# Kernel optimization log

Hardware: AMD Instinct MI355X
Metric: run time of the kernel (lower is better)

## Reference

```python
import jax, jax.numpy as jnp
import numpy as np

B, H = 16384, 1024
EPS = 1e-5


def setup_inputs() -> dict:
    key = jax.random.key(0)
    ks = jax.random.split(key, 12)
    inp = {
        "t": 0,
        "h": jax.random.normal(ks[0], (B, H), jnp.float32),
        "e": jax.random.normal(ks[1], (B, H), jnp.float32),
        # LiquidNeuron params
        "W_rec": jax.random.normal(ks[2], (H, H), jnp.float32) * 0.1,
        "bias": jnp.zeros((H,), jnp.float32),
        "tau": jnp.ones((H,), jnp.float32),
        "decay": jnp.ones((H,), jnp.float32),
        "ln_w": jnp.ones((H,), jnp.float32),
        "ln_b": jnp.zeros((H,), jnp.float32),
        # context_encoder: Linear -> ReLU -> Linear (dropout = identity in eval)
        "ce_w1": jax.random.normal(ks[3], (H, H), jnp.float32) * (1.0 / np.sqrt(H)),
        "ce_b1": jnp.zeros((H,), jnp.float32),
        "ce_w2": jax.random.normal(ks[4], (H, H), jnp.float32) * (1.0 / np.sqrt(H)),
        "ce_b2": jnp.zeros((H,), jnp.float32),
        # param_modulator
        "pm_w": jax.random.normal(ks[5], (H, H), jnp.float32) * (1.0 / np.sqrt(H)),
        "pm_b": jnp.zeros((H,), jnp.float32),
    }
    return inp


def reference(t, h, e, W_rec, bias, tau, decay, ln_w, ln_b,
              ce_w1, ce_b1, ce_w2, ce_b2, pm_w, pm_b):
    # context encoder (eval mode: dropout is identity)
    context = jnp.maximum(h @ ce_w1.T + ce_b1, 0.0) @ ce_w2.T + ce_b2  # [B,H]
    pa = context @ pm_w.T + pm_b  # param_adjustment [B,H]
    # bmm(e[:,None,:], (W_rec*(1+pa)[:,:,None]).T) == (1+pa) * (e @ W_rec.T)
    matmul_result = (1.0 + pa) * (e @ W_rec.T)  # [B,H]
    tau_adjusted = tau * jax.nn.sigmoid(pa)  # [B,H]
    dh_dt = (-decay * h + matmul_result + bias) / tau_adjusted
    # LayerNorm over last dim
    mu = jnp.mean(dh_dt, axis=-1, keepdims=True)
    var = jnp.var(dh_dt, axis=-1, keepdims=True)
    dh_dt = (dh_dt - mu) * jax.lax.rsqrt(var + EPS) * ln_w + ln_b
    return dh_dt
```

## Files before the change

kernel.cpp:

```cpp
#include <hip/hip_runtime.h>
#include <stdint.h>

#define H_DIM 1024
#define B_DIM 16384

typedef unsigned short u16;
typedef short bf16x8 __attribute__((ext_vector_type(8)));
typedef float f32x4 __attribute__((ext_vector_type(4)));

__device__ __forceinline__ u16 f2bf(float f) {
  union { float f; uint32_t u; } v; v.f = f;
  uint32_t r = v.u + 0x7fffu + ((v.u >> 16) & 1u);
  return (u16)(r >> 16);
}

#define GLDS16(gsrc, ldst)                                                                 \
  __builtin_amdgcn_global_load_lds((const __attribute__((address_space(1))) void*)(gsrc),  \
                                   (__attribute__((address_space(3))) void*)(ldst), 16, 0, 0)

__global__ __launch_bounds__(256) void cvt_f32_bf16(const float* __restrict__ in,
                                                    u16* __restrict__ out, int n4) {
  int i = blockIdx.x * blockDim.x + threadIdx.x;
  const int stride = gridDim.x * blockDim.x;
  const float4* __restrict__ in4 = (const float4*)in;
  ushort4* __restrict__ out4 = (ushort4*)out;
  for (; i < n4; i += stride) {
    float4 v = in4[i];
    ushort4 o;
    o.x = f2bf(v.x); o.y = f2bf(v.y); o.z = f2bf(v.z); o.w = f2bf(v.w);
    out4[i] = o;
  }
}


template <int MODE>
__device__ __forceinline__ void subtile_step(u16* shp, int slot, int slot2, int aoff, int boff,
                                             int wv, const u16*& pA0, const u16*& pA1,
                                             const u16*& pB0, const u16*& pB1,
                                             f32x4 (&acc)[8][4]) {
  const u16* Ab = shp + slot * 16384 + aoff;
  const u16* Bb = shp + slot * 16384 + 8192 + boff;
  bf16x8 aF[4], bF[4];
#pragma unroll
  for (int i = 0; i < 4; ++i) aF[i] = *(const bf16x8*)(Ab + i * 512);
#pragma unroll
  for (int i = 0; i < 4; ++i) bF[i] = *(const bf16x8*)(Bb + i * 512);
  if (MODE == 2) {
    u16* d = shp + slot2 * 16384 + wv * 1024;
    GLDS16(pA0, d); GLDS16(pA1, d + 512);
    pA0 += 32; pA1 += 32;
  }
  __builtin_amdgcn_s_barrier();
  asm volatile("s_waitcnt lgkmcnt(0)" ::: "memory");
  __builtin_amdgcn_s_setprio(1);
#pragma unroll
  for (int mf = 0; mf < 4; ++mf)
#pragma unroll
    for (int nf = 0; nf < 4; ++nf)
      acc[mf][nf] = __builtin_amdgcn_mfma_f32_16x16x32_bf16(aF[mf], bF[nf], acc[mf][nf], 0, 0, 0);
  __builtin_amdgcn_s_setprio(0);
  __builtin_amdgcn_s_barrier();
#pragma unroll
  for (int i = 0; i < 4; ++i) aF[i] = *(const bf16x8*)(Ab + (4 + i) * 512);
  if (MODE == 2) {
    u16* d = shp + slot2 * 16384 + 8192 + wv * 1024;
    GLDS16(pB0, d); GLDS16(pB1, d + 512);
    pB0 += 32; pB1 += 32;
  }
  __builtin_amdgcn_s_barrier();
  asm volatile("s_waitcnt lgkmcnt(0)" ::: "memory");
  __builtin_amdgcn_s_setprio(1);
#pragma unroll
  for (int mf = 0; mf < 4; ++mf)
#pragma unroll
    for (int nf = 0; nf < 4; ++nf)
      acc[4 + mf][nf] =
          __builtin_amdgcn_mfma_f32_16x16x32_bf16(aF[mf], bF[nf], acc[4 + mf][nf], 0, 0, 0);
  __builtin_amdgcn_s_setprio(0);
  if (MODE == 2) asm volatile("s_waitcnt vmcnt(4)" ::: "memory");
  if (MODE == 1) asm volatile("s_waitcnt vmcnt(0)" ::: "memory");
  __builtin_amdgcn_s_barrier();
}

template <bool RELU, bool HASBIAS, typename OUT>
__global__ __launch_bounds__(512, 2) void gemm256(const u16* __restrict__ A,
                                                  const u16* __restrict__ W,
                                                  const float* __restrict__ bias,
                                                  OUT* __restrict__ C) {
  extern __shared__ u16 sh[];
  const int t = threadIdx.x;
  const int wv = t >> 6, l = t & 63;
  const int wm = wv >> 2, wn = wv & 3;
  const int l15 = l & 15, lg = l >> 4;

  const int bid = blockIdx.x;
  const int logical = (bid & 7) * 32 + (bid >> 3);
  const int m0 = (logical >> 2) * 256;
  const int n0 = (logical & 3) * 256;

  const int koff = (lg ^ ((l15 >> 1) & 3)) * 8;
  const int aoff = (wm * 128 + l15) * 32 + koff;
  const int boff = (wn * 64 + l15) * 32 + koff;

  const int rowst = wv * 32 + (l >> 2);
  const int ksl = ((l & 3) ^ ((l >> 3) & 3)) * 8;
  const u16* pA0 = A + (size_t)(m0 + rowst) * H_DIM + ksl;
  const u16* pA1 = pA0 + 16 * H_DIM;
  const u16* pB0 = W + (size_t)(n0 + rowst) * H_DIM + ksl;
  const u16* pB1 = pB0 + 16 * H_DIM;

  f32x4 acc[8][4] = {};

  { u16* d = sh + wv * 1024;                 GLDS16(pA0, d); GLDS16(pA1, d + 512); pA0 += 32; pA1 += 32; }
  { u16* d = sh + 8192 + wv * 1024;          GLDS16(pB0, d); GLDS16(pB1, d + 512); pB0 += 32; pB1 += 32; }
  { u16* d = sh + 16384 + wv * 1024;         GLDS16(pA0, d); GLDS16(pA1, d + 512); pA0 += 32; pA1 += 32; }
  { u16* d = sh + 16384 + 8192 + wv * 1024;  GLDS16(pB0, d); GLDS16(pB1, d + 512); pB0 += 32; pB1 += 32; }
  asm volatile("s_waitcnt vmcnt(4)" ::: "memory");
  __builtin_amdgcn_s_barrier();

  for (int s = 0; s < 30; ++s)
    subtile_step<2>(sh, s & 3, (s + 2) & 3, aoff, boff, wv, pA0, pA1, pB0, pB1, acc);
  subtile_step<1>(sh, 2, 0, aoff, boff, wv, pA0, pA1, pB0, pB1, acc);
  subtile_step<0>(sh, 3, 0, aoff, boff, wv, pA0, pA1, pB0, pB1, acc);

  float bv[4];
#pragma unroll
  for (int nf = 0; nf < 4; ++nf)
    bv[nf] = HASBIAS ? bias[n0 + wn * 64 + nf * 16 + l15] : 0.0f;
#pragma unroll
  for (int mf = 0; mf < 8; ++mf) {
#pragma unroll
    for (int nf = 0; nf < 4; ++nf) {
      const int col = n0 + wn * 64 + nf * 16 + l15;
#pragma unroll
      for (int j = 0; j < 4; ++j) {
        const int row = m0 + wm * 128 + mf * 16 + lg * 4 + j;
        float v = acc[mf][nf][j] + bv[nf];
        if (RELU) v = fmaxf(v, 0.0f);
        if constexpr (sizeof(OUT) == 2)
          C[(size_t)row * H_DIM + col] = (OUT)f2bf(v);
        else
          C[(size_t)row * H_DIM + col] = v;
      }
    }
  }
}

__global__ __launch_bounds__(256) void liquid_ln(const float* __restrict__ h,
                                                 const float* __restrict__ pa,
                                                 const float* __restrict__ ev,
                                                 const float* __restrict__ bias,
                                                 const float* __restrict__ tau,
                                                 const float* __restrict__ decay,
                                                 const float* __restrict__ lnw,
                                                 const float* __restrict__ lnb,
                                                 float* __restrict__ out) {
  const int row = blockIdx.x;
  const int t = threadIdx.x;
  const size_t base = (size_t)row * H_DIM + t * 4;
  const int pcol = t * 4;

  float hf[4], pf[4], ef[4], bf_[4], tf[4], df[4];
  *(float4*)hf = *(const float4*)(h + base);
  *(float4*)pf = *(const float4*)(pa + base);
  *(float4*)ef = *(const float4*)(ev + base);
  *(float4*)bf_ = *(const float4*)(bias + pcol);
  *(float4*)tf = *(const float4*)(tau + pcol);
  *(float4*)df = *(const float4*)(decay + pcol);

  float d[4], s = 0.f, ss = 0.f;
#pragma unroll
  for (int j = 0; j < 4; ++j) {
    const float sig = 1.0f / (1.0f + __expf(-pf[j]));
    const float num = fmaf(-df[j], hf[j], fmaf(1.0f + pf[j], ef[j], bf_[j]));
    const float val = num / (tf[j] * sig);
    d[j] = val;
    s += val;
    ss += val * val;
  }
#pragma unroll
  for (int off = 32; off > 0; off >>= 1) {
    s += __shfl_down(s, off);
    ss += __shfl_down(ss, off);
  }
  __shared__ float rs[4], rss[4];
  const int wv = t >> 6;
  if ((t & 63) == 0) { rs[wv] = s; rss[wv] = ss; }
  __syncthreads();
  const float S = rs[0] + rs[1] + rs[2] + rs[3];
  const float SS = rss[0] + rss[1] + rss[2] + rss[3];
  const float mu = S * (1.0f / H_DIM);
  const float var = SS * (1.0f / H_DIM) - mu * mu;
  const float rstd = rsqrtf(var + 1e-5f);

  float lw[4], lb[4], o[4];
  *(float4*)lw = *(const float4*)(lnw + pcol);
  *(float4*)lb = *(const float4*)(lnb + pcol);
#pragma unroll
  for (int j = 0; j < 4; ++j) o[j] = fmaf((d[j] - mu) * rstd, lw[j], lb[j]);
  *(float4*)(out + base) = *(float4*)o;
}

extern "C" void kernel_launch(void* const* d_in, const int* in_sizes, int n_in,
                              void* d_out, int out_size, void* d_ws, size_t ws_size,
                              hipStream_t stream) {
  const float* h = (const float*)d_in[1];
  const float* e = (const float*)d_in[2];
  const float* Wrec = (const float*)d_in[3];
  const float* bias = (const float*)d_in[4];
  const float* tau = (const float*)d_in[5];
  const float* decay = (const float*)d_in[6];
  const float* lnw = (const float*)d_in[7];
  const float* lnb = (const float*)d_in[8];
  const float* ce_w1 = (const float*)d_in[9];
  const float* ce_b1 = (const float*)d_in[10];
  const float* ce_w2 = (const float*)d_in[11];
  const float* ce_b2 = (const float*)d_in[12];
  const float* pm_w = (const float*)d_in[13];
  const float* pm_b = (const float*)d_in[14];
  float* out = (float*)d_out;

  char* ws = (char*)d_ws;
  const size_t MB = 1024 * 1024;
  u16* w1b = (u16*)(ws + 0 * MB);
  u16* w2b = (u16*)(ws + 2 * MB);
  u16* w3b = (u16*)(ws + 4 * MB);
  u16* w4b = (u16*)(ws + 6 * MB);
  u16* ebf = (u16*)(ws + 8 * MB);
  u16* hbf = (u16*)(ws + 40 * MB);
  u16* t1 = (u16*)(ws + 72 * MB);
  u16* ctx = (u16*)(ws + 104 * MB);
  float* paf = (float*)(ws + 40 * MB);
  float* evf = (float*)(ws + 104 * MB);

  const int nBH4 = (B_DIM * H_DIM) / 4;
  const int nHH4 = (H_DIM * H_DIM) / 4;
  cvt_f32_bf16<<<2048, 256, 0, stream>>>(h, hbf, nBH4);
  cvt_f32_bf16<<<2048, 256, 0, stream>>>(e, ebf, nBH4);
  cvt_f32_bf16<<<512, 256, 0, stream>>>(ce_w1, w1b, nHH4);
  cvt_f32_bf16<<<512, 256, 0, stream>>>(ce_w2, w2b, nHH4);
  cvt_f32_bf16<<<512, 256, 0, stream>>>(pm_w, w3b, nHH4);
  cvt_f32_bf16<<<512, 256, 0, stream>>>(Wrec, w4b, nHH4);

  const int LDS_BYTES = 131072;
  hipFuncSetAttribute((const void*)gemm256<true, true, u16>,
                      hipFuncAttributeMaxDynamicSharedMemorySize, LDS_BYTES);
  hipFuncSetAttribute((const void*)gemm256<false, true, u16>,
                      hipFuncAttributeMaxDynamicSharedMemorySize, LDS_BYTES);
  hipFuncSetAttribute((const void*)gemm256<false, true, float>,
                      hipFuncAttributeMaxDynamicSharedMemorySize, LDS_BYTES);
  hipFuncSetAttribute((const void*)gemm256<false, false, float>,
                      hipFuncAttributeMaxDynamicSharedMemorySize, LDS_BYTES);

  const int NWG = (B_DIM / 256) * (H_DIM / 256);
  gemm256<true, true, u16><<<NWG, 512, LDS_BYTES, stream>>>(hbf, w1b, ce_b1, t1);
  gemm256<false, true, u16><<<NWG, 512, LDS_BYTES, stream>>>(t1, w2b, ce_b2, ctx);
  gemm256<false, true, float><<<NWG, 512, LDS_BYTES, stream>>>(ctx, w3b, pm_b, paf);
  gemm256<false, false, float><<<NWG, 512, LDS_BYTES, stream>>>(ebf, w4b, nullptr, evf);

  liquid_ln<<<B_DIM, 256, 0, stream>>>(h, paf, evf, bias, tau, decay, lnw, lnb, out);
}
```

Measured before the change: 251.2 us.

## Deepen GEMM prefetch to three stages, fuse weight casts, one-wave-per-row LayerNorm

The GEMM main loop now prefetches three K-slices ahead instead of two. It issues A and B loads together once per step and does all 32 MFMAs between a single pair of barriers, which removes the mid-step barrier and lgkmcnt wait. The four weight conversions are merged into one launch. The LayerNorm kernel maps one wavefront to each row and reduces with xor shuffles, so no shared-memory reduction or block sync is needed. Risks: more live fragment registers with 8 A fragments, and the removed lgkmcnt wait relies on the compiler to insert LDS read waits. Each LN lane's 16 contiguous floats are read as four float4 loads at a 64-byte lane stride, which is less coalesced.

```diff
diff --git a/kernel.cpp b/kernel.cpp
--- a/kernel.cpp
+++ b/kernel.cpp
@@ -32,51 +32,63 @@
   }
 }
 
+__global__ __launch_bounds__(256) void cvt4_f32_bf16(const float* __restrict__ a0,
+                                                     const float* __restrict__ a1,
+                                                     const float* __restrict__ a2,
+                                                     const float* __restrict__ a3,
+                                                     u16* __restrict__ o0, u16* __restrict__ o1,
+                                                     u16* __restrict__ o2, u16* __restrict__ o3) {
+  const int which = blockIdx.x >> 8;
+  const float* in = which == 0 ? a0 : which == 1 ? a1 : which == 2 ? a2 : a3;
+  u16* out = which == 0 ? o0 : which == 1 ? o1 : which == 2 ? o2 : o3;
+  const int n4 = (H_DIM * H_DIM) / 4;
+  int i = (blockIdx.x & 255) * 256 + threadIdx.x;
+  const float4* in4 = (const float4*)in;
+  ushort4* out4 = (ushort4*)out;
+  for (; i < n4; i += 256 * 256) {
+    float4 v = in4[i];
+    ushort4 o;
+    o.x = f2bf(v.x); o.y = f2bf(v.y); o.z = f2bf(v.z); o.w = f2bf(v.w);
+    out4[i] = o;
+  }
+}
+
 
 template <int MODE>
-__device__ __forceinline__ void subtile_step(u16* shp, int slot, int slot2, int aoff, int boff,
+__device__ __forceinline__ void subtile_step(u16* shp, int slot, int slot3, int aoff, int boff,
                                              int wv, const u16*& pA0, const u16*& pA1,
                                              const u16*& pB0, const u16*& pB1,
                                              f32x4 (&acc)[8][4]) {
   const u16* Ab = shp + slot * 16384 + aoff;
   const u16* Bb = shp + slot * 16384 + 8192 + boff;
-  bf16x8 aF[4], bF[4];
+  bf16x8 aF[8], bF[4];
 #pragma unroll
   for (int i = 0; i < 4; ++i) aF[i] = *(const bf16x8*)(Ab + i * 512);
 #pragma unroll
   for (int i = 0; i < 4; ++i) bF[i] = *(const bf16x8*)(Bb + i * 512);
-  if (MODE == 2) {
-    u16* d = shp + slot2 * 16384 + wv * 1024;
-    GLDS16(pA0, d); GLDS16(pA1, d + 512);
-    pA0 += 32; pA1 += 32;
+#pragma unroll
+  for (int i = 4; i < 8; ++i) aF[i] = *(const bf16x8*)(Ab + i * 512);
+  if (MODE == 3) {
+    u16* da = shp + slot3 * 16384 + wv * 1024;
+    GLDS16(pA0, da); GLDS16(pA1, da + 512);
+    u16* db = shp + slot3 * 16384 + 8192 + wv * 1024;
+    GLDS16(pB0, db); GLDS16(pB1, db + 512);
+    pA0 += 32; pA1 += 32; pB0 += 32; pB1 += 32;
   }
   __builtin_amdgcn_s_barrier();
-  asm volatile("s_waitcnt lgkmcnt(0)" ::: "memory");
   __builtin_amdgcn_s_setprio(1);
 #pragma unroll
   for (int mf = 0; mf < 4; ++mf)
+#pragma unroll
+    for (int nf = 0; nf < 4; ++nf)
+      acc[mf][nf] = __builtin_amdgcn_mfma_f32_16x16x32_bf16(aF[mf], bF[nf], acc[mf][nf], 0, 0, 0);
+#pragma unroll
+  for (int mf = 4; mf < 8; ++mf)
 #pragma unroll
     for (int nf = 0; nf < 4; ++nf)
       acc[mf][nf] = __builtin_amdgcn_mfma_f32_16x16x32_bf16(aF[mf], bF[nf], acc[mf][nf], 0, 0, 0);
   __builtin_amdgcn_s_setprio(0);
-  __builtin_amdgcn_s_barrier();
-#pragma unroll
-  for (int i = 0; i < 4; ++i) aF[i] = *(const bf16x8*)(Ab + (4 + i) * 512);
-  if (MODE == 2) {
-    u16* d = shp + slot2 * 16384 + 8192 + wv * 1024;
-    GLDS16(pB0, d); GLDS16(pB1, d + 512);
-    pB0 += 32; pB1 += 32;
-  }
-  __builtin_amdgcn_s_barrier();
-  asm volatile("s_waitcnt lgkmcnt(0)" ::: "memory");
-  __builtin_amdgcn_s_setprio(1);
-#pragma unroll
-  for (int mf = 0; mf < 4; ++mf)
-#pragma unroll
-    for (int nf = 0; nf < 4; ++nf)
-      acc[4 + mf][nf] =
-          __builtin_amdgcn_mfma_f32_16x16x32_bf16(aF[mf], bF[nf], acc[4 + mf][nf], 0, 0, 0);
-  __builtin_amdgcn_s_setprio(0);
+  if (MODE == 3) asm volatile("s_waitcnt vmcnt(8)" ::: "memory");
   if (MODE == 2) asm volatile("s_waitcnt vmcnt(4)" ::: "memory");
   if (MODE == 1) asm volatile("s_waitcnt vmcnt(0)" ::: "memory");
   __builtin_amdgcn_s_barrier();
@@ -111,15 +123,20 @@
 
   f32x4 acc[8][4] = {};
 
-  { u16* d = sh + wv * 1024;                 GLDS16(pA0, d); GLDS16(pA1, d + 512); pA0 += 32; pA1 += 32; }
-  { u16* d = sh + 8192 + wv * 1024;          GLDS16(pB0, d); GLDS16(pB1, d + 512); pB0 += 32; pB1 += 32; }
-  { u16* d = sh + 16384 + wv * 1024;         GLDS16(pA0, d); GLDS16(pA1, d + 512); pA0 += 32; pA1 += 32; }
-  { u16* d = sh + 16384 + 8192 + wv * 1024;  GLDS16(pB0, d); GLDS16(pB1, d + 512); pB0 += 32; pB1 += 32; }
-  asm volatile("s_waitcnt vmcnt(4)" ::: "memory");
+#pragma unroll
+  for (int s = 0; s < 3; ++s) {
+    u16* da = sh + s * 16384 + wv * 1024;
+    GLDS16(pA0, da); GLDS16(pA1, da + 512);
+    u16* db = sh + s * 16384 + 8192 + wv * 1024;
+    GLDS16(pB0, db); GLDS16(pB1, db + 512);
+    pA0 += 32; pA1 += 32; pB0 += 32; pB1 += 32;
+  }
+  asm volatile("s_waitcnt vmcnt(8)" ::: "memory");
   __builtin_amdgcn_s_barrier();
 
-  for (int s = 0; s < 30; ++s)
-    subtile_step<2>(sh, s & 3, (s + 2) & 3, aoff, boff, wv, pA0, pA1, pB0, pB1, acc);
+  for (int s = 0; s < 29; ++s)
+    subtile_step<3>(sh, s & 3, (s + 3) & 3, aoff, boff, wv, pA0, pA1, pB0, pB1, acc);
+  subtile_step<2>(sh, 1, 0, aoff, boff, wv, pA0, pA1, pB0, pB1, acc);
   subtile_step<1>(sh, 2, 0, aoff, boff, wv, pA0, pA1, pB0, pB1, acc);
   subtile_step<0>(sh, 3, 0, aoff, boff, wv, pA0, pA1, pB0, pB1, acc);
 
@@ -155,50 +172,50 @@
                                                  const float* __restrict__ lnw,
                                                  const float* __restrict__ lnb,
                                                  float* __restrict__ out) {
-  const int row = blockIdx.x;
-  const int t = threadIdx.x;
-  const size_t base = (size_t)row * H_DIM + t * 4;
-  const int pcol = t * 4;
-
-  float hf[4], pf[4], ef[4], bf_[4], tf[4], df[4];
-  *(float4*)hf = *(const float4*)(h + base);
-  *(float4*)pf = *(const float4*)(pa + base);
-  *(float4*)ef = *(const float4*)(ev + base);
-  *(float4*)bf_ = *(const float4*)(bias + pcol);
-  *(float4*)tf = *(const float4*)(tau + pcol);
-  *(float4*)df = *(const float4*)(decay + pcol);
-
-  float d[4], s = 0.f, ss = 0.f;
-#pragma unroll
-  for (int j = 0; j < 4; ++j) {
-    const float sig = 1.0f / (1.0f + __expf(-pf[j]));
-    const float num = fmaf(-df[j], hf[j], fmaf(1.0f + pf[j], ef[j], bf_[j]));
-    const float val = num / (tf[j] * sig);
-    d[j] = val;
-    s += val;
-    ss += val * val;
-  }
-#pragma unroll
-  for (int off = 32; off > 0; off >>= 1) {
-    s += __shfl_down(s, off);
-    ss += __shfl_down(ss, off);
-  }
-  __shared__ float rs[4], rss[4];
-  const int wv = t >> 6;
-  if ((t & 63) == 0) { rs[wv] = s; rss[wv] = ss; }
-  __syncthreads();
-  const float S = rs[0] + rs[1] + rs[2] + rs[3];
-  const float SS = rss[0] + rss[1] + rss[2] + rss[3];
-  const float mu = S * (1.0f / H_DIM);
-  const float var = SS * (1.0f / H_DIM) - mu * mu;
+  const int wv = threadIdx.x >> 6, l = threadIdx.x & 63;
+  const int row = blockIdx.x * 4 + wv;
+  const size_t base = (size_t)row * H_DIM + l * 16;
+  const int pc = l * 16;
+
+  float d[16];
+  float s = 0.f, ss = 0.f;
+#pragma unroll
+  for (int c = 0; c < 4; ++c) {
+    float hf[4], pf[4], ef[4], bf_[4], tf[4], df[4];
+    *(float4*)hf = *(const float4*)(h + base + c * 4);
+    *(float4*)pf = *(const float4*)(pa + base + c * 4);
+    *(float4*)ef = *(const float4*)(ev + base + c * 4);
+    *(float4*)bf_ = *(const float4*)(bias + pc + c * 4);
+    *(float4*)tf = *(const float4*)(tau + pc + c * 4);
+    *(float4*)df = *(const float4*)(decay + pc + c * 4);
+#pragma unroll
+    for (int j = 0; j < 4; ++j) {
+      const float sig = 1.0f / (1.0f + __expf(-pf[j]));
+      const float num = fmaf(-df[j], hf[j], fmaf(1.0f + pf[j], ef[j], bf_[j]));
+      const float val = num / (tf[j] * sig);
+      d[c * 4 + j] = val;
+      s += val;
+      ss += val * val;
+    }
+  }
+#pragma unroll
+  for (int off = 32; off; off >>= 1) {
+    s += __shfl_xor(s, off);
+    ss += __shfl_xor(ss, off);
+  }
+  const float mu = s * (1.0f / H_DIM);
+  const float var = ss * (1.0f / H_DIM) - mu * mu;
   const float rstd = rsqrtf(var + 1e-5f);
 
-  float lw[4], lb[4], o[4];
-  *(float4*)lw = *(const float4*)(lnw + pcol);
-  *(float4*)lb = *(const float4*)(lnb + pcol);
-#pragma unroll
-  for (int j = 0; j < 4; ++j) o[j] = fmaf((d[j] - mu) * rstd, lw[j], lb[j]);
-  *(float4*)(out + base) = *(float4*)o;
+#pragma unroll
+  for (int c = 0; c < 4; ++c) {
+    float lw[4], lb[4], o[4];
+    *(float4*)lw = *(const float4*)(lnw + pc + c * 4);
+    *(float4*)lb = *(const float4*)(lnb + pc + c * 4);
+#pragma unroll
+    for (int j = 0; j < 4; ++j) o[j] = fmaf((d[c * 4 + j] - mu) * rstd, lw[j], lb[j]);
+    *(float4*)(out + base + c * 4) = *(float4*)o;
+  }
 }
 
 extern "C" void kernel_launch(void* const* d_in, const int* in_sizes, int n_in,
@@ -234,13 +251,9 @@
   float* evf = (float*)(ws + 104 * MB);
 
   const int nBH4 = (B_DIM * H_DIM) / 4;
-  const int nHH4 = (H_DIM * H_DIM) / 4;
   cvt_f32_bf16<<<2048, 256, 0, stream>>>(h, hbf, nBH4);
   cvt_f32_bf16<<<2048, 256, 0, stream>>>(e, ebf, nBH4);
-  cvt_f32_bf16<<<512, 256, 0, stream>>>(ce_w1, w1b, nHH4);
-  cvt_f32_bf16<<<512, 256, 0, stream>>>(ce_w2, w2b, nHH4);
-  cvt_f32_bf16<<<512, 256, 0, stream>>>(pm_w, w3b, nHH4);
-  cvt_f32_bf16<<<512, 256, 0, stream>>>(Wrec, w4b, nHH4);
+  cvt4_f32_bf16<<<1024, 256, 0, stream>>>(ce_w1, ce_w2, pm_w, Wrec, w1b, w2b, w3b, w4b);
 
   const int LDS_BYTES = 131072;
   hipFuncSetAttribute((const void*)gemm256<true, true, u16>,
@@ -258,5 +271,5 @@
   gemm256<false, true, float><<<NWG, 512, LDS_BYTES, stream>>>(ctx, w3b, pm_b, paf);
   gemm256<false, false, float><<<NWG, 512, LDS_BYTES, stream>>>(ebf, w4b, nullptr, evf);
 
-  liquid_ln<<<B_DIM, 256, 0, stream>>>(h, paf, evf, bias, tau, decay, lnw, lnb, out);
-}
+  liquid_ln<<<B_DIM / 4, 256, 0, stream>>>(h, paf, evf, bias, tau, decay, lnw, lnb, out);
+}
```

Result: slower. 266.8 us (+6.2%).
